# Performance work log

Measured on AMD Instinct MI355X. Metric: run time of the kernel, lower is better.

## Reference

```python
import jax, jax.numpy as jnp
from jax import lax
import numpy as np

OBS_DIM, POP_DIM, ACT_DIM, DE_POP = 256, 10, 8, 10
HID1, HID2 = 256, 256
SPIKE_TS = 25
ENC_VTH = 0.999
CDECAY = 0.5
VDECAY = 0.75
VTH_TEMPORAL = 0.5  # NEURON_VTH_*_temporal stays at its init value 0.5
GRAD_WIN = 0.5


@jax.custom_vjp
def enc_spike(v):
    return (v > ENC_VTH).astype(v.dtype)

def _es_fwd(v):
    return enc_spike(v), None

def _es_bwd(_, g):
    return (g,)  # straight-through

enc_spike.defvjp(_es_fwd, _es_bwd)


@jax.custom_vjp
def rect_spike(v, vth):
    return (v > vth).astype(v.dtype)

def _rs_fwd(v, vth):
    return rect_spike(v, vth), (v, vth)

def _rs_bwd(res, g):
    v, vth = res
    # rectangular pseudo-gradient window; vth is detached in the original (numpy roundtrip)
    return (g * (jnp.abs(v - vth) < GRAD_WIN).astype(g.dtype), jnp.zeros_like(vth))

rect_spike.defvjp(_rs_fwd, _rs_bwd)


def setup_inputs() -> dict:
    key = jax.random.key(0)
    ks = jax.random.split(key, 10)
    B = 2048
    obs = jax.random.normal(ks[0], (B, OBS_DIM), dtype=jnp.float32)
    # encoder Gaussian receptive-field params
    enc_mean = jnp.broadcast_to(jnp.linspace(-3.0, 3.0, POP_DIM, dtype=jnp.float32), (1, OBS_DIM, POP_DIM))
    enc_std = jnp.full((1, OBS_DIM, POP_DIM), 0.15, dtype=jnp.float32)
    n_in = OBS_DIM * POP_DIM
    out_pop = ACT_DIM * DE_POP
    w1 = jax.random.normal(ks[1], (HID1, n_in), dtype=jnp.float32) / np.sqrt(n_in)
    b1 = jnp.zeros((HID1,), dtype=jnp.float32)
    w2 = jax.random.normal(ks[2], (HID2, HID1), dtype=jnp.float32) / np.sqrt(HID1)
    b2 = jnp.zeros((HID2,), dtype=jnp.float32)
    w3 = jax.random.normal(ks[3], (out_pop, HID2), dtype=jnp.float32) / np.sqrt(HID2)
    b3 = jnp.zeros((out_pop,), dtype=jnp.float32)
    dec_w = jax.random.normal(ks[4], (ACT_DIM, DE_POP), dtype=jnp.float32) / np.sqrt(DE_POP)
    dec_b = jnp.zeros((ACT_DIM,), dtype=jnp.float32)
    return {"obs": obs, "enc_mean": enc_mean, "enc_std": enc_std,
            "w1": w1, "b1": b1, "w2": w2, "b2": b2, "w3": w3, "b3": b3,
            "dec_w": dec_w, "dec_b": dec_b, "batch_size": B}


def _forward(obs, enc_mean, enc_std, w1, b1, w2, b2, w3, b3, dec_w, dec_b):
    B = obs.shape[0]
    # --- population encoder: Gaussian receptive fields -> regular spike train ---
    pop_act = jnp.exp(-0.5 * (obs[:, :, None] - enc_mean) ** 2 / (enc_std ** 2))
    pop_act = pop_act.reshape(B, OBS_DIM * POP_DIM)  # [B, N]

    def enc_step(volt, _):
        volt = volt + pop_act
        s = enc_spike(volt)
        return volt - s * ENC_VTH, s

    _, in_spikes = lax.scan(enc_step, jnp.zeros_like(pop_act), None, length=SPIKE_TS)  # [T, B, N]

    # --- spike MLP with LIF neurons and dynamic threshold ---
    def lif_dth(x, W, b, state):
        c, v_prev, s = state
        c = c * CDECAY + x @ W.T + b
        v = v_prev * VDECAY * (1.0 - s) + c
        # dynamic threshold (detached in original via numpy roundtrip)
        vth = lax.stop_gradient(0.5 * VTH_TEMPORAL + 0.5 * (jnp.exp((v_prev - v) / 3.0) - 1.0))
        s = rect_spike(v, vth)
        return (c, v, s)

    def zeros_state(n):
        z = jnp.zeros((B, n), dtype=obs.dtype)
        return (z, z, z)

    init = (zeros_state(HID1), zeros_state(HID2), zeros_state(ACT_DIM * DE_POP))

    def mlp_step(states, x):
        s1 = lif_dth(x, w1, b1, states[0])
        s2 = lif_dth(s1[2], w2, b2, states[1])
        s3 = lif_dth(s2[2], w3, b3, states[2])
        return (s1, s2, s3), s3[2]

    _, out_spikes = lax.scan(mlp_step, init, in_spikes)  # [T, B, out_pop]
    pop_out = out_spikes.sum(axis=0) / SPIKE_TS  # rate decode

    # --- decoder: grouped Conv1d(kernel=pop_dim) == per-action dot product, then tanh ---
    raw = jnp.einsum('bap,ap->ba', pop_out.reshape(B, ACT_DIM, DE_POP), dec_w) + dec_b
    return jnp.tanh(raw)


def reference(obs, enc_mean, enc_std, w1, b1, w2, b2, w3, b3, dec_w, dec_b, batch_size):
    return _forward(obs, enc_mean, enc_std, w1, b1, w2, b2, w3, b3, dec_w, dec_b)
```

## Files before the change

### kernel.cpp

```cpp
#include <hip/hip_runtime.h>
#include <stdint.h>

#define NB 2048
#define OBSD 256
#define POP 10
#define NIN 2560
#define H 256
#define OUTP 80
#define TS 25
#define CAP 256
#define RING 12

typedef __attribute__((ext_vector_type(2))) float f2;
typedef __attribute__((address_space(1))) void gas_void;
typedef __attribute__((address_space(3))) void las_void;

__device__ __forceinline__ float exp_cr(float x) {
    return (float)exp((double)x);
}

__device__ __forceinline__ int rfl(int v) {
    return __builtin_amdgcn_readfirstlane(v);
}

__device__ __forceinline__ void gload_lds4(const float* g, float* l) {
    __builtin_amdgcn_global_load_lds((gas_void*)g, (las_void*)l, 4, 0, 0);
}

#define VM_FENCE8 do { asm volatile("s_waitcnt vmcnt(8)"); __builtin_amdgcn_sched_barrier(0); } while (0)
#define VM_FENCE0 do { asm volatile("s_waitcnt vmcnt(0)"); __builtin_amdgcn_sched_barrier(0); } while (0)

struct Acc25 {
    f2 p[12];
    float last;
};

__device__ __forceinline__ void acc_zero(Acc25& a) {
    #pragma unroll
    for (int i = 0; i < 12; ++i) { a.p[i].x = 0.0f; a.p[i].y = 0.0f; }
    a.last = 0.0f;
}

__device__ __forceinline__ void acc_fold(Acc25& acc, Acc25& part) {
    #pragma unroll
    for (int i = 0; i < 12; ++i) {
        acc.p[i].x = __fadd_rn(acc.p[i].x, part.p[i].x);
        acc.p[i].y = __fadd_rn(acc.p[i].y, part.p[i].y);
        part.p[i].x = 0.0f; part.p[i].y = 0.0f;
    }
    acc.last = __fadd_rn(acc.last, part.last);
    part.last = 0.0f;
}

__device__ __forceinline__ void acc_unpack(const Acc25& a, float* __restrict__ t) {
    #pragma unroll
    for (int i = 0; i < 12; ++i) { t[2 * i] = a.p[i].x; t[2 * i + 1] = a.p[i].y; }
    t[24] = a.last;
}

__device__ __forceinline__ void fma25(float w, const float* __restrict__ rec, float lastv, Acc25& a) {
    f2 wp; wp.x = w; wp.y = w;
    float4 q[6];
    #pragma unroll
    for (int i = 0; i < 6; ++i) q[i] = ((const float4*)rec)[i];
    const f2* r2 = (const f2*)q;
    #pragma unroll
    for (int i = 0; i < 12; ++i) {
#if __has_builtin(__builtin_elementwise_fma)
        a.p[i] = __builtin_elementwise_fma(wp, r2[i], a.p[i]);
#else
        a.p[i].x = fmaf(w, r2[i].x, a.p[i].x);
        a.p[i].y = fmaf(w, r2[i].y, a.p[i].y);
#endif
    }
    a.last = fmaf(w, lastv, a.last);
}

__device__ __forceinline__ void write_rec(float* __restrict__ recs, float* __restrict__ rec24,
                                          int pos, uint32_t m) {
    float4* dst = (float4*)&recs[pos * 24];
    #pragma unroll
    for (int p = 0; p < 6; ++p) {
        float4 v;
        v.x = (m >> (4 * p)) & 1u ? 1.0f : 0.0f;
        v.y = (m >> (4 * p + 1)) & 1u ? 1.0f : 0.0f;
        v.z = (m >> (4 * p + 2)) & 1u ? 1.0f : 0.0f;
        v.w = (m >> (4 * p + 3)) & 1u ? 1.0f : 0.0f;
        dst[p] = v;
    }
    rec24[pos] = (m >> 24) & 1u ? 1.0f : 0.0f;
}

#define WALK_RING(CNT, WT, DOFOLD, TGT)                                         \
  do {                                                                          \
    const int _n = (CNT);                                                       \
    _Pragma("unroll")                                                           \
    for (int _r = 0; _r < 8; ++_r) {                                            \
      int _ip = rfl(idxL[_r]);                                                  \
      gload_lds4((WT) + _ip + tid, &wring[wave][_r][0]);                        \
    }                                                                           \
    int _cs = 0, _is = 8;                                                       \
    int _j = 0;                                                                 \
    for (; _j + 4 <= _n; _j += 4) {                                             \
      _Pragma("unroll")                                                         \
      for (int _r = 0; _r < 4; ++_r) {                                          \
        int _ip = rfl(idxL[_j + 8 + _r]);                                       \
        int _sl = _is + _r;  _sl = (_sl >= RING) ? _sl - RING : _sl;            \
        gload_lds4((WT) + _ip + tid, &wring[wave][_sl][0]);                     \
      }                                                                         \
      VM_FENCE8;                                                                \
      _Pragma("unroll")                                                         \
      for (int _r = 0; _r < 4; ++_r) {                                          \
        int _row = _j + _r;                                                     \
        int _ii = rfl(idxL[_row]);                                              \
        int _sc = _cs + _r;  _sc = (_sc >= RING) ? _sc - RING : _sc;            \
        float _wv = wring[wave][_sc][lane];                                     \
        if (DOFOLD) { while (_ii >= nextB) { acc_fold(acc, part); nextB += 320 * H; } } \
        fma25(_wv, &recs[_row * 24], rec24[_row], TGT);                         \
      }                                                                         \
      _cs += 4; if (_cs >= RING) _cs -= RING;                                   \
      _is += 4; if (_is >= RING) _is -= RING;                                   \
    }                                                                           \
    VM_FENCE0;                                                                  \
    for (; _j < _n; ++_j) {                \
      int _ii = rfl(idxL[_j]);                                                  \
      float _wv = wring[wave][_cs][lane];                                       \
      _cs += 1; if (_cs >= RING) _cs -= RING;                                   \
      if (DOFOLD) { while (_ii >= nextB) { acc_fold(acc, part); nextB += 320 * H; } } \
      fma25(_wv, &recs[_j * 24], rec24[_j], TGT);                               \
    }                                                                           \
  } while (0)

__global__ __launch_bounds__(256) void k0_transpose(
    const float* __restrict__ w1, const float* __restrict__ w2, const float* __restrict__ w3,
    float* __restrict__ w1t, float* __restrict__ w2t, float* __restrict__ w3t)
{
    __shared__ float tile[32][33];
    int bid = blockIdx.x;
    const float* src; float* dst; int R, C, tr, tc;
    if (bid < 640)      { src = w1; dst = w1t; R = 256; C = NIN; tr = bid / 80; tc = bid % 80; }
    else if (bid < 704) { int t = bid - 640; src = w2; dst = w2t; R = 256; C = 256; tr = t / 8; tc = t % 8; }
    else                { int t = bid - 704; src = w3; dst = w3t; R = OUTP; C = 256; tr = t / 8; tc = t % 8; }
    const int tx = threadIdx.x & 31, ty = threadIdx.x >> 5;
    const int r0 = tr * 32, c0 = tc * 32;
    #pragma unroll
    for (int i = 0; i < 4; ++i) {
        int r = r0 + ty + i * 8, c = c0 + tx;
        if (r < R && c < C) tile[ty + i * 8][tx] = src[r * C + c];
    }
    __syncthreads();
    #pragma unroll
    for (int i = 0; i < 4; ++i) {
        int c = c0 + ty + i * 8, r = r0 + tx;
        if (c < C && r < R) dst[c * R + r] = tile[tx][ty + i * 8];
    }
}

__device__ __forceinline__ void lif_step(float x, float bv, float& c, float& v, float& s) {
    float cn = __fadd_rn(__fadd_rn(__fmul_rn(c, 0.5f), x), bv);
    c = cn;
    float vp = v;
    float t  = __fmul_rn(__fmul_rn(vp, 0.75f), __fadd_rn(1.0f, -s));
    float vn = __fadd_rn(t, cn);
    float d  = __fadd_rn(vp, -vn);
    v = vn;
    float ag_f  = __fmul_rn(d, 0.33333334f);
    float ex_a  = __expf(ag_f);
    float vth_a = 0.25f + 0.5f * (ex_a - 1.0f);
    float delta = (1e-5f + 1e-6f * fabsf(ag_f)) * (ex_a + fabsf(vth_a) + 1.0f);
    if (vn > vth_a + delta) {
        s = 1.0f;
    } else if (vn < vth_a - delta) {
        s = 0.0f;
    } else {
        float ag  = __fdiv_rn(d, 3.0f);
        float ex  = exp_cr(ag);
        float vth = __fadd_rn(0.25f, __fmul_rn(0.5f, __fadd_rn(ex, -1.0f)));
        s = (vn > vth) ? 1.0f : 0.0f;
    }
}

__global__ __launch_bounds__(256, 4) void k1_fused(
    const float* __restrict__ obs, const float* __restrict__ emean, const float* __restrict__ estd,
    const float* __restrict__ w1t, const float* __restrict__ w2t, const float* __restrict__ w3t,
    const float* __restrict__ b1, const float* __restrict__ b2, const float* __restrict__ b3,
    const float* __restrict__ dw, const float* __restrict__ db, float* __restrict__ out)
{
    __shared__ __align__(16) float recs[CAP * 24];
    __shared__ float rec24[CAP];
    __shared__ int   idxL[CAP + 8];
    __shared__ __align__(16) float wring[4][RING][64];
    __shared__ uint32_t cntA[40];
    __shared__ uint32_t waveCnt[4];
    __shared__ float cnt3[OUTP];

    const int tid = threadIdx.x;
    const int wave = tid >> 6, lane = tid & 63;
    const int b = blockIdx.x;
    const unsigned long long below = (1ull << lane) - 1ull;

    uint32_t msk[10];
    #pragma unroll
    for (int k = 0; k < 10; ++k) {
        int i = k * 256 + tid;
        int o = i / 10;
        float x  = obs[b * OBSD + o];
        float mu = emean[i];
        float sd = estd[i];
        float dd = __fadd_rn(x, -mu);
        float d2 = __fmul_rn(dd, dd);
        float nm = __fmul_rn(-0.5f, d2);
        float dn = __fmul_rn(sd, sd);
        float arg = __fdiv_rn(nm, dn);
        uint32_t m = 0;
        if (arg >= -3.23f) {
            float a  = exp_cr(arg);
            float volt = 0.0f;
            #pragma unroll
            for (int t = 0; t < TS; ++t) {
                volt = __fadd_rn(volt, a);
                if (volt > 0.999f) { m |= (1u << t); volt = __fadd_rn(volt, -0.999f); }
            }
        }
        msk[k] = m;
    }
    #pragma unroll
    for (int k = 0; k < 10; ++k) {
        unsigned long long bal = __ballot(msk[k] != 0u);
        if (lane == 0) cntA[k * 4 + wave] = (uint32_t)__popcll(bal);
    }
    __syncthreads();

    Acc25 acc, part;
    acc_zero(acc); acc_zero(part);
    int nextB = 320 * H;
    int run = 0;
    #pragma unroll
    for (int k = 0; k < 10; ++k) {
        if (k == 5) {
            if (tid < 8) idxL[run + tid] = 0;
            __syncthreads();
            WALK_RING(run, w1t, 1, part);
            __syncthreads();
            run = 0;
        }
        int tot = 0, pre = 0;
        #pragma unroll
        for (int w = 0; w < 4; ++w) {
            int c = (int)cntA[k * 4 + w];
            tot += c;
            if (w < wave) pre += c;
        }
        uint32_t m = msk[k];
        unsigned long long bal = __ballot(m != 0u);
        if (m) {
            int pos = run + pre + (int)__popcll(bal & below);
            idxL[pos] = (k * 256 + tid) * H;
            write_rec(recs, rec24, pos, m);
        }
        run += tot;
    }
    if (tid < 8) idxL[run + tid] = 0;
    __syncthreads();
    WALK_RING(run, w1t, 1, part);
    acc_fold(acc, part);

    uint32_t m1 = 0;
    {
        float cur[TS];
        acc_unpack(acc, cur);
        const float b1v = b1[tid];
        float c1 = 0, v1 = 0, s1 = 0;
        #pragma unroll
        for (int t = 0; t < TS; ++t) {
            lif_step(cur[t], b1v, c1, v1, s1);
            if (s1 != 0.0f) m1 |= (1u << t);
        }
    }
    unsigned long long bal1 = __ballot(m1 != 0u);
    if (lane == 0) waveCnt[wave] = (uint32_t)__popcll(bal1);
    __syncthreads();
    int base1 = 0, n1 = 0;
    #pragma unroll
    for (int w = 0; w < 4; ++w) {
        if (w < wave) base1 += (int)waveCnt[w];
        n1 += (int)waveCnt[w];
    }
    if (m1) {
        int pos = base1 + (int)__popcll(bal1 & below);
        idxL[pos] = tid * H;
        write_rec(recs, rec24, pos, m1);
    }
    if (tid < 8) idxL[n1 + tid] = 0;
    __syncthreads();

    Acc25 acc2;
    acc_zero(acc2);
    WALK_RING(n1, w2t, 0, acc2);
    uint32_t m2 = 0;
    {
        float cur[TS];
        acc_unpack(acc2, cur);
        const float b2v = b2[tid];
        float c2 = 0, v2 = 0, s2 = 0;
        #pragma unroll
        for (int t = 0; t < TS; ++t) {
            lif_step(cur[t], b2v, c2, v2, s2);
            if (s2 != 0.0f) m2 |= (1u << t);
        }
    }
    unsigned long long bal2 = __ballot(m2 != 0u);
    if (lane == 0) waveCnt[wave] = (uint32_t)__popcll(bal2);
    __syncthreads();
    int base2 = 0, n2 = 0;
    #pragma unroll
    for (int w = 0; w < 4; ++w) {
        if (w < wave) base2 += (int)waveCnt[w];
        n2 += (int)waveCnt[w];
    }
    if (m2) {
        int pos = base2 + (int)__popcll(bal2 & below);
        idxL[pos] = tid * OUTP;
        write_rec(recs, rec24, pos, m2);
    }
    if (tid < 8) idxL[n2 + tid] = 0;
    __syncthreads();

    if (tid < OUTP) {
        Acc25 x3;
        acc_zero(x3);
        WALK_RING(n2, w3t, 0, x3);
        float cur[TS];
        acc_unpack(x3, cur);
        const float b3v = b3[tid];
        float c3 = 0, v3 = 0, s3 = 0, ct = 0;
        #pragma unroll
        for (int t = 0; t < TS; ++t) {
            lif_step(cur[t], b3v, c3, v3, s3);
            ct += s3;
        }
        cnt3[tid] = ct;
    }
    __syncthreads();

    if (tid < 8) {
        float raw = 0.0f;
        #pragma unroll
        for (int pp = 0; pp < POP; ++pp) {
            float po = __fdiv_rn(cnt3[tid * POP + pp], 25.0f);
            raw = __fadd_rn(raw, __fmul_rn(po, dw[tid * POP + pp]));
        }
        raw = __fadd_rn(raw, db[tid]);
        out[b * 8 + tid] = (float)tanh((double)raw);
    }
}

extern "C" void kernel_launch(void* const* d_in, const int* in_sizes, int n_in,
                              void* d_out, int out_size, void* d_ws, size_t ws_size,
                              hipStream_t stream) {
    const float* obs   = (const float*)d_in[0];
    const float* emean = (const float*)d_in[1];
    const float* estd  = (const float*)d_in[2];
    const float* w1    = (const float*)d_in[3];
    const float* b1    = (const float*)d_in[4];
    const float* w2    = (const float*)d_in[5];
    const float* b2    = (const float*)d_in[6];
    const float* w3    = (const float*)d_in[7];
    const float* b3    = (const float*)d_in[8];
    const float* dw    = (const float*)d_in[9];
    const float* db    = (const float*)d_in[10];
    float* out = (float*)d_out;

    char* ws = (char*)d_ws;
    float* w1t = (float*)(ws);
    float* w2t = (float*)(ws + 2621440);
    float* w3t = (float*)(ws + 2883584);

    k0_transpose<<<728, 256, 0, stream>>>(w1, w2, w3, w1t, w2t, w3t);
    k1_fused<<<NB, 256, 0, stream>>>(obs, emean, estd, w1t, w2t, w3t,
                                     b1, b2, b3, dw, db, out);
}
```

Baseline: 421.7 us.

## Replace LDS ring prefetch with register prefetch and process two rows per block

Removes the global_load_lds ring buffer and its vmcnt fences. The weight-row walk now prefetches the next four weight values into registers, one group ahead. Each block now loops over two batch rows, so the grid is halved to 1024 blocks, and launch bounds rise to 5 waves per SIMD. The goal is to cut LDS use and async-copy synchronisation and to amortise block launch cost. The trade-offs are shallower prefetch depth, possible register pressure, and serialisation of two rows inside one block.

```diff
diff --git a/kernel.cpp b/kernel.cpp
--- a/kernel.cpp
+++ b/kernel.cpp
@@ -9,11 +9,8 @@
 #define OUTP 80
 #define TS 25
 #define CAP 256
-#define RING 12
 
 typedef __attribute__((ext_vector_type(2))) float f2;
-typedef __attribute__((address_space(1))) void gas_void;
-typedef __attribute__((address_space(3))) void las_void;
 
 __device__ __forceinline__ float exp_cr(float x) {
     return (float)exp((double)x);
@@ -22,13 +19,6 @@
 __device__ __forceinline__ int rfl(int v) {
     return __builtin_amdgcn_readfirstlane(v);
 }
-
-__device__ __forceinline__ void gload_lds4(const float* g, float* l) {
-    __builtin_amdgcn_global_load_lds((gas_void*)g, (las_void*)l, 4, 0, 0);
-}
-
-#define VM_FENCE8 do { asm volatile("s_waitcnt vmcnt(8)"); __builtin_amdgcn_sched_barrier(0); } while (0)
-#define VM_FENCE0 do { asm volatile("s_waitcnt vmcnt(0)"); __builtin_amdgcn_sched_barrier(0); } while (0)
 
 struct Acc25 {
     f2 p[12];
@@ -91,44 +81,37 @@
     rec24[pos] = (m >> 24) & 1u ? 1.0f : 0.0f;
 }
 
-#define WALK_RING(CNT, WT, DOFOLD, TGT)                                         \
-  do {                                                                          \
-    const int _n = (CNT);                                                       \
-    _Pragma("unroll")                                                           \
-    for (int _r = 0; _r < 8; ++_r) {                                            \
-      int _ip = rfl(idxL[_r]);                                                  \
-      gload_lds4((WT) + _ip + tid, &wring[wave][_r][0]);                        \
-    }                                                                           \
-    int _cs = 0, _is = 8;                                                       \
-    int _j = 0;                                                                 \
-    for (; _j + 4 <= _n; _j += 4) {                                             \
-      _Pragma("unroll")                                                         \
-      for (int _r = 0; _r < 4; ++_r) {                                          \
-        int _ip = rfl(idxL[_j + 8 + _r]);                                       \
-        int _sl = _is + _r;  _sl = (_sl >= RING) ? _sl - RING : _sl;            \
-        gload_lds4((WT) + _ip + tid, &wring[wave][_sl][0]);                     \
-      }                                                                         \
-      VM_FENCE8;                                                                \
-      _Pragma("unroll")                                                         \
-      for (int _r = 0; _r < 4; ++_r) {                                          \
-        int _row = _j + _r;                                                     \
-        int _ii = rfl(idxL[_row]);                                              \
-        int _sc = _cs + _r;  _sc = (_sc >= RING) ? _sc - RING : _sc;            \
-        float _wv = wring[wave][_sc][lane];                                     \
-        if (DOFOLD) { while (_ii >= nextB) { acc_fold(acc, part); nextB += 320 * H; } } \
-        fma25(_wv, &recs[_row * 24], rec24[_row], TGT);                         \
-      }                                                                         \
-      _cs += 4; if (_cs >= RING) _cs -= RING;                                   \
-      _is += 4; if (_is >= RING) _is -= RING;                                   \
-    }                                                                           \
-    VM_FENCE0;                                                                  \
-    for (; _j < _n; ++_j) {                \
-      int _ii = rfl(idxL[_j]);                                                  \
-      float _wv = wring[wave][_cs][lane];                                       \
-      _cs += 1; if (_cs >= RING) _cs -= RING;                                   \
+#define WALK_BODY(CNT, WT, DOFOLD, TGT)                                        \
+  do {                                                                         \
+    const int _n = (CNT);                                                      \
+    int _pi0 = 0, _pi1 = 0, _pi2 = 0, _pi3 = 0;                                \
+    float _pw0 = 0, _pw1 = 0, _pw2 = 0, _pw3 = 0;                              \
+    if (_n > 0) { _pi0 = rfl(idxL[0]); _pw0 = (WT)[_pi0 + tid]; }              \
+    if (_n > 1) { _pi1 = rfl(idxL[1]); _pw1 = (WT)[_pi1 + tid]; }              \
+    if (_n > 2) { _pi2 = rfl(idxL[2]); _pw2 = (WT)[_pi2 + tid]; }              \
+    if (_n > 3) { _pi3 = rfl(idxL[3]); _pw3 = (WT)[_pi3 + tid]; }              \
+    int _j = 0;                                                                \
+    for (; _j + 4 <= _n; _j += 4) {                                            \
+      int _c0 = _pi0, _c1 = _pi1, _c2 = _pi2, _c3 = _pi3;                      \
+      float _w0 = _pw0, _w1 = _pw1, _w2 = _pw2, _w3 = _pw3;                    \
+      if (_j + 4 < _n) { _pi0 = rfl(idxL[_j + 4]); _pw0 = (WT)[_pi0 + tid]; }  \
+      if (_j + 5 < _n) { _pi1 = rfl(idxL[_j + 5]); _pw1 = (WT)[_pi1 + tid]; }  \
+      if (_j + 6 < _n) { _pi2 = rfl(idxL[_j + 6]); _pw2 = (WT)[_pi2 + tid]; }  \
+      if (_j + 7 < _n) { _pi3 = rfl(idxL[_j + 7]); _pw3 = (WT)[_pi3 + tid]; }  \
+      if (DOFOLD) { while (_c0 >= nextB) { acc_fold(acc, part); nextB += 320 * H; } } \
+      fma25(_w0, &recs[_j * 24], rec24[_j], TGT);                              \
+      if (DOFOLD) { while (_c1 >= nextB) { acc_fold(acc, part); nextB += 320 * H; } } \
+      fma25(_w1, &recs[(_j + 1) * 24], rec24[_j + 1], TGT);                    \
+      if (DOFOLD) { while (_c2 >= nextB) { acc_fold(acc, part); nextB += 320 * H; } } \
+      fma25(_w2, &recs[(_j + 2) * 24], rec24[_j + 2], TGT);                    \
+      if (DOFOLD) { while (_c3 >= nextB) { acc_fold(acc, part); nextB += 320 * H; } } \
+      fma25(_w3, &recs[(_j + 3) * 24], rec24[_j + 3], TGT);                    \
+    }                                                                          \
+    for (; _j < _n; ++_j) {                          \
+      int _ii = rfl(idxL[_j]); float _wv = (WT)[_ii + tid];                    \
       if (DOFOLD) { while (_ii >= nextB) { acc_fold(acc, part); nextB += 320 * H; } } \
-      fma25(_wv, &recs[_j * 24], rec24[_j], TGT);                               \
-    }                                                                           \
+      fma25(_wv, &recs[_j * 24], rec24[_j], TGT);                              \
+    }                                                                          \
   } while (0)
 
 __global__ __launch_bounds__(256) void k0_transpose(
@@ -180,7 +163,7 @@
     }
 }
 
-__global__ __launch_bounds__(256, 4) void k1_fused(
+__global__ __launch_bounds__(256, 5) void k1_fused(
     const float* __restrict__ obs, const float* __restrict__ emean, const float* __restrict__ estd,
     const float* __restrict__ w1t, const float* __restrict__ w2t, const float* __restrict__ w3t,
     const float* __restrict__ b1, const float* __restrict__ b2, const float* __restrict__ b3,
@@ -188,170 +171,170 @@
 {
     __shared__ __align__(16) float recs[CAP * 24];
     __shared__ float rec24[CAP];
-    __shared__ int   idxL[CAP + 8];
-    __shared__ __align__(16) float wring[4][RING][64];
+    __shared__ int   idxL[CAP];
     __shared__ uint32_t cntA[40];
     __shared__ uint32_t waveCnt[4];
     __shared__ float cnt3[OUTP];
 
     const int tid = threadIdx.x;
     const int wave = tid >> 6, lane = tid & 63;
-    const int b = blockIdx.x;
     const unsigned long long below = (1ull << lane) - 1ull;
 
-    uint32_t msk[10];
-    #pragma unroll
-    for (int k = 0; k < 10; ++k) {
-        int i = k * 256 + tid;
-        int o = i / 10;
-        float x  = obs[b * OBSD + o];
-        float mu = emean[i];
-        float sd = estd[i];
-        float dd = __fadd_rn(x, -mu);
-        float d2 = __fmul_rn(dd, dd);
-        float nm = __fmul_rn(-0.5f, d2);
-        float dn = __fmul_rn(sd, sd);
-        float arg = __fdiv_rn(nm, dn);
-        uint32_t m = 0;
-        if (arg >= -3.23f) {
-            float a  = exp_cr(arg);
-            float volt = 0.0f;
+    #pragma unroll 1
+    for (int rr = 0; rr < 2; ++rr) {
+        const int b = (blockIdx.x << 1) | rr;
+        if (rr) __syncthreads();
+
+        uint32_t msk[10];
+        #pragma unroll
+        for (int k = 0; k < 10; ++k) {
+            int i = k * 256 + tid;
+            int o = i / 10;
+            float x  = obs[b * OBSD + o];
+            float mu = emean[i];
+            float sd = estd[i];
+            float dd = __fadd_rn(x, -mu);
+            float d2 = __fmul_rn(dd, dd);
+            float nm = __fmul_rn(-0.5f, d2);
+            float dn = __fmul_rn(sd, sd);
+            float arg = __fdiv_rn(nm, dn);
+            uint32_t m = 0;
+            if (arg >= -3.23f) {
+                float a  = exp_cr(arg);
+                float volt = 0.0f;
+                #pragma unroll
+                for (int t = 0; t < TS; ++t) {
+                    volt = __fadd_rn(volt, a);
+                    if (volt > 0.999f) { m |= (1u << t); volt = __fadd_rn(volt, -0.999f); }
+                }
+            }
+            msk[k] = m;
+        }
+        #pragma unroll
+        for (int k = 0; k < 10; ++k) {
+            unsigned long long bal = __ballot(msk[k] != 0u);
+            if (lane == 0) cntA[k * 4 + wave] = (uint32_t)__popcll(bal);
+        }
+        __syncthreads();
+
+        Acc25 acc, part;
+        acc_zero(acc); acc_zero(part);
+        int nextB = 320 * H;
+        int run = 0;
+        #pragma unroll
+        for (int k = 0; k < 10; ++k) {
+            if (k == 5) {
+                __syncthreads();
+                WALK_BODY(run, w1t, 1, part);
+                __syncthreads();
+                run = 0;
+            }
+            int tot = 0, pre = 0;
+            #pragma unroll
+            for (int w = 0; w < 4; ++w) {
+                int c = (int)cntA[k * 4 + w];
+                tot += c;
+                if (w < wave) pre += c;
+            }
+            uint32_t m = msk[k];
+            unsigned long long bal = __ballot(m != 0u);
+            if (m) {
+                int pos = run + pre + (int)__popcll(bal & below);
+                idxL[pos] = (k * 256 + tid) * H;
+                write_rec(recs, rec24, pos, m);
+            }
+            run += tot;
+        }
+        __syncthreads();
+        WALK_BODY(run, w1t, 1, part);
+        acc_fold(acc, part);
+
+        uint32_t m1 = 0;
+        {
+            float cur[TS];
+            acc_unpack(acc, cur);
+            const float b1v = b1[tid];
+            float c1 = 0, v1 = 0, s1 = 0;
             #pragma unroll
             for (int t = 0; t < TS; ++t) {
-                volt = __fadd_rn(volt, a);
-                if (volt > 0.999f) { m |= (1u << t); volt = __fadd_rn(volt, -0.999f); }
-            }
-        }
-        msk[k] = m;
-    }
-    #pragma unroll
-    for (int k = 0; k < 10; ++k) {
-        unsigned long long bal = __ballot(msk[k] != 0u);
-        if (lane == 0) cntA[k * 4 + wave] = (uint32_t)__popcll(bal);
-    }
-    __syncthreads();
-
-    Acc25 acc, part;
-    acc_zero(acc); acc_zero(part);
-    int nextB = 320 * H;
-    int run = 0;
-    #pragma unroll
-    for (int k = 0; k < 10; ++k) {
-        if (k == 5) {
-            if (tid < 8) idxL[run + tid] = 0;
-            __syncthreads();
-            WALK_RING(run, w1t, 1, part);
-            __syncthreads();
-            run = 0;
-        }
-        int tot = 0, pre = 0;
+                lif_step(cur[t], b1v, c1, v1, s1);
+                if (s1 != 0.0f) m1 |= (1u << t);
+            }
+        }
+        unsigned long long bal1 = __ballot(m1 != 0u);
+        if (lane == 0) waveCnt[wave] = (uint32_t)__popcll(bal1);
+        __syncthreads();
+        int base1 = 0, n1 = 0;
         #pragma unroll
         for (int w = 0; w < 4; ++w) {
-            int c = (int)cntA[k * 4 + w];
-            tot += c;
-            if (w < wave) pre += c;
-        }
-        uint32_t m = msk[k];
-        unsigned long long bal = __ballot(m != 0u);
-        if (m) {
-            int pos = run + pre + (int)__popcll(bal & below);
-            idxL[pos] = (k * 256 + tid) * H;
-            write_rec(recs, rec24, pos, m);
-        }
-        run += tot;
-    }
-    if (tid < 8) idxL[run + tid] = 0;
-    __syncthreads();
-    WALK_RING(run, w1t, 1, part);
-    acc_fold(acc, part);
-
-    uint32_t m1 = 0;
-    {
-        float cur[TS];
-        acc_unpack(acc, cur);
-        const float b1v = b1[tid];
-        float c1 = 0, v1 = 0, s1 = 0;
-        #pragma unroll
-        for (int t = 0; t < TS; ++t) {
-            lif_step(cur[t], b1v, c1, v1, s1);
-            if (s1 != 0.0f) m1 |= (1u << t);
-        }
-    }
-    unsigned long long bal1 = __ballot(m1 != 0u);
-    if (lane == 0) waveCnt[wave] = (uint32_t)__popcll(bal1);
-    __syncthreads();
-    int base1 = 0, n1 = 0;
-    #pragma unroll
-    for (int w = 0; w < 4; ++w) {
-        if (w < wave) base1 += (int)waveCnt[w];
-        n1 += (int)waveCnt[w];
-    }
-    if (m1) {
-        int pos = base1 + (int)__popcll(bal1 & below);
-        idxL[pos] = tid * H;
-        write_rec(recs, rec24, pos, m1);
-    }
-    if (tid < 8) idxL[n1 + tid] = 0;
-    __syncthreads();
-
-    Acc25 acc2;
-    acc_zero(acc2);
-    WALK_RING(n1, w2t, 0, acc2);
-    uint32_t m2 = 0;
-    {
-        float cur[TS];
-        acc_unpack(acc2, cur);
-        const float b2v = b2[tid];
-        float c2 = 0, v2 = 0, s2 = 0;
-        #pragma unroll
-        for (int t = 0; t < TS; ++t) {
-            lif_step(cur[t], b2v, c2, v2, s2);
-            if (s2 != 0.0f) m2 |= (1u << t);
-        }
-    }
-    unsigned long long bal2 = __ballot(m2 != 0u);
-    if (lane == 0) waveCnt[wave] = (uint32_t)__popcll(bal2);
-    __syncthreads();
-    int base2 = 0, n2 = 0;
-    #pragma unroll
-    for (int w = 0; w < 4; ++w) {
-        if (w < wave) base2 += (int)waveCnt[w];
-        n2 += (int)waveCnt[w];
-    }
-    if (m2) {
-        int pos = base2 + (int)__popcll(bal2 & below);
-        idxL[pos] = tid * OUTP;
-        write_rec(recs, rec24, pos, m2);
-    }
-    if (tid < 8) idxL[n2 + tid] = 0;
-    __syncthreads();
-
-    if (tid < OUTP) {
-        Acc25 x3;
-        acc_zero(x3);
-        WALK_RING(n2, w3t, 0, x3);
-        float cur[TS];
-        acc_unpack(x3, cur);
-        const float b3v = b3[tid];
-        float c3 = 0, v3 = 0, s3 = 0, ct = 0;
-        #pragma unroll
-        for (int t = 0; t < TS; ++t) {
-            lif_step(cur[t], b3v, c3, v3, s3);
-            ct += s3;
-        }
-        cnt3[tid] = ct;
-    }
-    __syncthreads();
-
-    if (tid < 8) {
-        float raw = 0.0f;
-        #pragma unroll
-        for (int pp = 0; pp < POP; ++pp) {
-            float po = __fdiv_rn(cnt3[tid * POP + pp], 25.0f);
-            raw = __fadd_rn(raw, __fmul_rn(po, dw[tid * POP + pp]));
-        }
-        raw = __fadd_rn(raw, db[tid]);
-        out[b * 8 + tid] = (float)tanh((double)raw);
+            if (w < wave) base1 += (int)waveCnt[w];
+            n1 += (int)waveCnt[w];
+        }
+        if (m1) {
+            int pos = base1 + (int)__popcll(bal1 & below);
+            idxL[pos] = tid * H;
+            write_rec(recs, rec24, pos, m1);
+        }
+        __syncthreads();
+
+        Acc25 acc2;
+        acc_zero(acc2);
+        WALK_BODY(n1, w2t, 0, acc2);
+        uint32_t m2 = 0;
+        {
+            float cur[TS];
+            acc_unpack(acc2, cur);
+            const float b2v = b2[tid];
+            float c2 = 0, v2 = 0, s2 = 0;
+            #pragma unroll
+            for (int t = 0; t < TS; ++t) {
+                lif_step(cur[t], b2v, c2, v2, s2);
+                if (s2 != 0.0f) m2 |= (1u << t);
+            }
+        }
+        unsigned long long bal2 = __ballot(m2 != 0u);
+        if (lane == 0) waveCnt[wave] = (uint32_t)__popcll(bal2);
+        __syncthreads();
+        int base2 = 0, n2 = 0;
+        #pragma unroll
+        for (int w = 0; w < 4; ++w) {
+            if (w < wave) base2 += (int)waveCnt[w];
+            n2 += (int)waveCnt[w];
+        }
+        if (m2) {
+            int pos = base2 + (int)__popcll(bal2 & below);
+            idxL[pos] = tid * OUTP;
+            write_rec(recs, rec24, pos, m2);
+        }
+        __syncthreads();
+
+        if (tid < OUTP) {
+            Acc25 x3;
+            acc_zero(x3);
+            WALK_BODY(n2, w3t, 0, x3);
+            float cur[TS];
+            acc_unpack(x3, cur);
+            const float b3v = b3[tid];
+            float c3 = 0, v3 = 0, s3 = 0, ct = 0;
+            #pragma unroll
+            for (int t = 0; t < TS; ++t) {
+                lif_step(cur[t], b3v, c3, v3, s3);
+                ct += s3;
+            }
+            cnt3[tid] = ct;
+        }
+        __syncthreads();
+
+        if (tid < 8) {
+            float raw = 0.0f;
+            #pragma unroll
+            for (int pp = 0; pp < POP; ++pp) {
+                float po = __fdiv_rn(cnt3[tid * POP + pp], 25.0f);
+                raw = __fadd_rn(raw, __fmul_rn(po, dw[tid * POP + pp]));
+            }
+            raw = __fadd_rn(raw, db[tid]);
+            out[b * 8 + tid] = (float)tanh((double)raw);
+        }
     }
 }
 
@@ -377,6 +360,6 @@
     float* w3t = (float*)(ws + 2883584);
 
     k0_transpose<<<728, 256, 0, stream>>>(w1, w2, w3, w1t, w2t, w3t);
-    k1_fused<<<NB, 256, 0, stream>>>(obs, emean, estd, w1t, w2t, w3t,
-                                     b1, b2, b3, dw, db, out);
-}
+    k1_fused<<<1024, 256, 0, stream>>>(obs, emean, estd, w1t, w2t, w3t,
+                                       b1, b2, b3, dw, db, out);
+}
```

Measured after the change: 451.3 us. 7.0% more time.
